# Kernel tuning notes

Hardware: AMD Instinct MI355X
Metric: run time of the kernel (lower is better)

Reference implementation:

```python
import jax, jax.numpy as jnp
import numpy as np

B, S, D_IN, D_OUT = 4, 2048, 4096, 16384


def setup_inputs() -> dict:
    key = jax.random.key(0)
    k1, k2, k3, k4 = jax.random.split(key, 4)
    x = jax.random.normal(k1, (B, S, D_IN), dtype=jnp.float32)
    # per-channel symmetric int8 weights, [out_features, in_features]
    weight_int8 = jax.random.randint(k2, (D_OUT, D_IN), -128, 128, dtype=jnp.int32).astype(jnp.int8)
    # per-channel weight scales (positive, realistic magnitude)
    weight_scale = jax.random.uniform(k3, (D_OUT,), dtype=jnp.float32) * 0.01 + 1e-4
    # static per-tensor activation scale (calibrated constant)
    act_scale = jnp.float32(0.02)
    bias = jax.random.normal(k4, (D_OUT,), dtype=jnp.float32) * 0.1
    return {"x": x, "weight_int8": weight_int8, "weight_scale": weight_scale,
            "act_scale": act_scale, "bias": bias}


def reference(x, weight_int8, weight_scale, act_scale, bias):
    orig_shape = x.shape
    orig_dtype = x.dtype
    x2d = x.reshape(-1, orig_shape[-1])  # [M, D_in]
    # static per-tensor symmetric activation quantization
    x_int8 = jnp.clip(jnp.round(x2d.astype(jnp.float32) / act_scale), -128, 127).astype(jnp.int8)
    y_int32 = jnp.matmul(x_int8, weight_int8.T, preferred_element_type=jnp.int32)  # [M, D_out]
    output_scale = (act_scale * weight_scale).astype(jnp.float32)  # [D_out]
    y = y_int32.astype(jnp.float32) * output_scale[None, :] + bias.astype(jnp.float32)[None, :]
    return y.reshape(*orig_shape[:-1], y.shape[-1]).astype(orig_dtype)
```

## Files before the change

### kernel.cpp

```cpp
#include <hip/hip_runtime.h>
#include <stdint.h>

#define GAS __attribute__((address_space(1)))
#define LAS __attribute__((address_space(3)))

typedef int v4i __attribute__((ext_vector_type(4)));

constexpr int Mdim = 8192;
constexpr int Ndim = 16384;
constexpr int Kdim = 4096;

__device__ __forceinline__ int pack4i8(int a, int b, int c, int d) {
    return (a & 255) | ((b & 255) << 8) | ((c & 255) << 16) | ((d & 255) << 24);
}

__device__ __forceinline__ int qz(float v, float inv) {
    return (int)fminf(fmaxf(rintf(v * inv), -128.0f), 127.0f);
}

__global__ void k_quant_x(const float* __restrict__ x, const float* __restrict__ asc,
                          int8_t* __restrict__ xq) {
    const int i = blockIdx.x * blockDim.x + threadIdx.x;
    const float inv = 1.0f / *asc;
    const float4* xv = (const float4*)x + (size_t)i * 4;
    float4 f0 = xv[0], f1 = xv[1], f2 = xv[2], f3 = xv[3];
    int4 o;
    o.x = pack4i8(qz(f0.x, inv), qz(f0.y, inv), qz(f0.z, inv), qz(f0.w, inv));
    o.y = pack4i8(qz(f1.x, inv), qz(f1.y, inv), qz(f1.z, inv), qz(f1.w, inv));
    o.z = pack4i8(qz(f2.x, inv), qz(f2.y, inv), qz(f2.z, inv), qz(f2.w, inv));
    o.w = pack4i8(qz(f3.x, inv), qz(f3.y, inv), qz(f3.z, inv), qz(f3.w, inv));
    ((int4*)xq)[i] = o;
}

__global__ void k_conv_w(const int* __restrict__ w, int8_t* __restrict__ wq) {
    const int i = blockIdx.x * blockDim.x + threadIdx.x;
    const int4* wv = (const int4*)w + (size_t)i * 4;
    int4 a = wv[0], b = wv[1], c = wv[2], d = wv[3];
    int4 o;
    o.x = pack4i8(a.x, a.y, a.z, a.w);
    o.y = pack4i8(b.x, b.y, b.z, b.w);
    o.z = pack4i8(c.x, c.y, c.z, c.w);
    o.w = pack4i8(d.x, d.y, d.z, d.w);
    ((int4*)wq)[i] = o;
}

constexpr int NSTEP = Kdim / 64;

__global__ __launch_bounds__(512, 2)
void k_gemm256(const int8_t* __restrict__ Aq, const int8_t* __restrict__ Bq,
               const float* __restrict__ wscale, const float* __restrict__ asc,
               const float* __restrict__ bias, float* __restrict__ out) {
    __shared__ __align__(16) int8_t lds[131072];
    const int tid = threadIdx.x, lane = tid & 63, w = tid >> 6;
    const int wm = w >> 2, wn = w & 3;
    const int lrow = lane & 15, kgrp = lane >> 4;

    const int bid = blockIdx.x;
    const int swz = ((bid & 7) << 8) | (bid >> 3);
    const int mt = swz & 31, nt = swz >> 5;
    const int m0 = mt << 8, n0 = nt << 8;

    const int srow = (w << 4) + (lane >> 2);
    const int scol = (((lane & 3) ^ ((lane >> 3) & 3)) << 4);
    const int8_t* pA0 = Aq + (size_t)(m0 + srow) * Kdim + scol;
    const int8_t* pA1 = pA0 + (size_t)128 * Kdim;
    const int8_t* pB0 = Bq + (size_t)(n0 + srow) * Kdim + scol;
    const int8_t* pB1 = pB0 + (size_t)128 * Kdim;
    const int dstoff = w << 10;

    auto stage = [&](int slot, int kb) {
        int8_t* ba = lds + (slot << 14) + dstoff;
        int8_t* bb = lds + 65536 + (slot << 14) + dstoff;
        __builtin_amdgcn_global_load_lds((const GAS void*)(pB0 + kb), (LAS void*)bb, 16, 0, 0);
        __builtin_amdgcn_global_load_lds((const GAS void*)(pB1 + kb), (LAS void*)(bb + 8192), 16, 0, 0);
        __builtin_amdgcn_global_load_lds((const GAS void*)(pA0 + kb), (LAS void*)ba, 16, 0, 0);
        __builtin_amdgcn_global_load_lds((const GAS void*)(pA1 + kb), (LAS void*)(ba + 8192), 16, 0, 0);
    };

    const int kc = (kgrp ^ ((lrow >> 1) & 3)) << 4;
    const int arowb = (((wm << 7) + lrow) << 6) + kc;
    const int browb = (((wn << 6) + lrow) << 6) + kc;

    auto readfr = [&](int slot, v4i* a, v4i* b) {
        const int8_t* As_ = lds + (slot << 14);
        const int8_t* Bs_ = lds + 65536 + (slot << 14);
#pragma unroll
        for (int f = 0; f < 4; ++f)
            b[f] = *(const v4i*)(Bs_ + browb + f * 1024);
#pragma unroll
        for (int f = 0; f < 8; ++f)
            a[f] = *(const v4i*)(As_ + arowb + f * 1024);
    };

    v4i acc[8][4];
#pragma unroll
    for (int i = 0; i < 8; ++i)
#pragma unroll
        for (int j = 0; j < 4; ++j) acc[i][j] = (v4i){0, 0, 0, 0};

    auto domfma = [&](v4i* a, v4i* b) {
        __builtin_amdgcn_s_setprio(1);
#pragma unroll
        for (int fi = 0; fi < 8; ++fi)
#pragma unroll
            for (int fj = 0; fj < 4; ++fj)
                acc[fi][fj] = __builtin_amdgcn_mfma_i32_16x16x64_i8(a[fi], b[fj], acc[fi][fj], 0, 0, 0);
        __builtin_amdgcn_s_setprio(0);
    };

    v4i aP[8], bP[4], aQ[8], bQ[4];

    stage(0, 0); stage(1, 64); stage(2, 128);
    asm volatile("s_waitcnt vmcnt(8)" ::: "memory");
    __builtin_amdgcn_s_barrier();
    readfr(0, aP, bP);

    int kb = 192;
    for (int s = 0; s < NSTEP; s += 2) {
        if (s < NSTEP - 1) {
            if (s == NSTEP - 2) asm volatile("s_waitcnt vmcnt(0)" ::: "memory");
            else                asm volatile("s_waitcnt vmcnt(4)" ::: "memory");
            __builtin_amdgcn_s_barrier();
            readfr((s + 1) & 3, aQ, bQ);
            if (s < NSTEP - 3) { stage((s + 3) & 3, kb); kb += 64; }
        }
        domfma(aP, bP);
        const int t = s + 1;
        if (t < NSTEP - 1) {
            asm volatile("s_waitcnt vmcnt(4)" ::: "memory");
            __builtin_amdgcn_s_barrier();
            readfr((t + 1) & 3, aP, bP);
            if (t < NSTEP - 3) { stage((t + 3) & 3, kb); kb += 64; }
        }
        domfma(aQ, bQ);
    }

    const float ascale = *asc;
#pragma unroll
    for (int fj = 0; fj < 4; ++fj) {
        const int col = n0 + (wn << 6) + fj * 16 + lrow;
        const float sc = ascale * wscale[col];
        const float bb = bias[col];
#pragma unroll
        for (int mi = 0; mi < 8; ++mi) {
            const int r0 = m0 + (wm << 7) + mi * 16 + (kgrp << 2);
            float* o = out + (size_t)r0 * Ndim + col;
#pragma unroll
            for (int q = 0; q < 4; ++q)
                o[(size_t)q * Ndim] = (float)acc[mi][fj][q] * sc + bb;
        }
    }
}

template <bool AQ, bool BQ>
__global__ __launch_bounds__(256)
void k_gemm(const int8_t* __restrict__ Aq, const float* __restrict__ Xf,
            const int8_t* __restrict__ Bq, const int* __restrict__ W32,
            const float* __restrict__ wscale, const float* __restrict__ asc,
            const float* __restrict__ bias, float* __restrict__ out) {
    constexpr int BM = 128, BN = 128, BK = 64;
    constexpr int KT = Kdim / BK;
    __shared__ __align__(16) int8_t As[2][BM * BK];
    __shared__ __align__(16) int8_t Bs[2][BN * BK];

    const int tid  = threadIdx.x;
    const int lane = tid & 63;
    const int wid  = tid >> 6;
    const int wm = wid >> 1, wn = wid & 1;
    const int lrow = lane & 15, kgrp = lane >> 4;

    const int cpx = gridDim.x >> 3;
    const int swz = ((int)blockIdx.x & 7) * cpx + ((int)blockIdx.x >> 3);
    const int mt = swz & (Mdim / BM - 1);
    const int nt = swz / (Mdim / BM);
    const int m0 = mt * BM, n0 = nt * BN;

    const float ascale = *asc;
    const float inv = 1.0f / ascale;

    v4i acc[4][4];
#pragma unroll
    for (int i = 0; i < 4; ++i)
#pragma unroll
        for (int j = 0; j < 4; ++j) acc[i][j] = (v4i){0, 0, 0, 0};

    auto stage = [&](int buf, int kt) {
        const int k0 = kt * BK;
        if constexpr (AQ) {
            int8_t* ldsp = &As[buf][wid << 10];
            const int8_t* g = Aq + (size_t)(m0 + (tid >> 2)) * Kdim + k0 + ((tid & 3) << 4);
            __builtin_amdgcn_global_load_lds((const GAS void*)g, (LAS void*)ldsp, 16, 0, 0);
            __builtin_amdgcn_global_load_lds((const GAS void*)(g + (size_t)64 * Kdim),
                                             (LAS void*)(ldsp + 4096), 16, 0, 0);
        } else {
            const int row = tid >> 1, cb = (tid & 1) << 5;
            const float4* src = (const float4*)(Xf + (size_t)(m0 + row) * Kdim + k0 + cb);
            int t[8];
#pragma unroll
            for (int j = 0; j < 8; ++j) {
                float4 f = src[j];
                t[j] = pack4i8(qz(f.x, inv), qz(f.y, inv), qz(f.z, inv), qz(f.w, inv));
            }
            int4* dst = (int4*)&As[buf][row * BK + cb];
            dst[0] = make_int4(t[0], t[1], t[2], t[3]);
            dst[1] = make_int4(t[4], t[5], t[6], t[7]);
        }
        if constexpr (BQ) {
            int8_t* ldsp = &Bs[buf][wid << 10];
            const int8_t* g = Bq + (size_t)(n0 + (tid >> 2)) * Kdim + k0 + ((tid & 3) << 4);
            __builtin_amdgcn_global_load_lds((const GAS void*)g, (LAS void*)ldsp, 16, 0, 0);
            __builtin_amdgcn_global_load_lds((const GAS void*)(g + (size_t)64 * Kdim),
                                             (LAS void*)(ldsp + 4096), 16, 0, 0);
        } else {
            const int row = tid >> 1, cb = (tid & 1) << 5;
            const int4* src = (const int4*)(W32 + (size_t)(n0 + row) * Kdim + k0 + cb);
            int t[8];
#pragma unroll
            for (int j = 0; j < 8; ++j) {
                int4 vv = src[j];
                t[j] = pack4i8(vv.x, vv.y, vv.z, vv.w);
            }
            int4* dst = (int4*)&Bs[buf][row * BK + cb];
            dst[0] = make_int4(t[0], t[1], t[2], t[3]);
            dst[1] = make_int4(t[4], t[5], t[6], t[7]);
        }
    };

    stage(0, 0);
    for (int kt = 0; kt < KT; ++kt) {
        const int cur = kt & 1;
        __syncthreads();
        if (kt + 1 < KT) stage(cur ^ 1, kt + 1);

        v4i a[4], b[4];
        const int koff = kgrp << 4;
#pragma unroll
        for (int i = 0; i < 4; ++i) {
            a[i] = *(const v4i*)&As[cur][(wm * 64 + i * 16 + lrow) * BK + koff];
            b[i] = *(const v4i*)&Bs[cur][(wn * 64 + i * 16 + lrow) * BK + koff];
        }
#pragma unroll
        for (int i = 0; i < 4; ++i)
#pragma unroll
            for (int j = 0; j < 4; ++j)
                acc[i][j] = __builtin_amdgcn_mfma_i32_16x16x64_i8(a[i], b[j], acc[i][j], 0, 0, 0);
    }

#pragma unroll
    for (int j = 0; j < 4; ++j) {
        const int col = n0 + wn * 64 + j * 16 + lrow;
        const float sc = ascale * wscale[col];
        const float bb = bias[col];
#pragma unroll
        for (int i = 0; i < 4; ++i) {
            const int r0 = m0 + wm * 64 + i * 16 + (kgrp << 2);
            float* o = out + (size_t)r0 * Ndim + col;
#pragma unroll
            for (int r = 0; r < 4; ++r)
                o[(size_t)r * Ndim] = (float)acc[i][j][r] * sc + bb;
        }
    }
}

extern "C" void kernel_launch(void* const* d_in, const int* in_sizes, int n_in,
                              void* d_out, int out_size, void* d_ws, size_t ws_size,
                              hipStream_t stream) {
    const float* x      = (const float*)d_in[0];
    const int*   w32    = (const int*)d_in[1];
    const float* wscale = (const float*)d_in[2];
    const float* asc    = (const float*)d_in[3];
    const float* bias   = (const float*)d_in[4];
    float* out = (float*)d_out;

    const size_t nx = (size_t)Mdim * Kdim;
    const size_t nw = (size_t)Ndim * Kdim;
    int8_t* xq = (int8_t*)d_ws;
    int8_t* wq = xq + nx;

    const bool haveX = ws_size >= nx;
    const bool haveW = ws_size >= nx + nw;

    if (haveX) k_quant_x<<<(int)(nx / 16 / 256), 256, 0, stream>>>(x, asc, xq);
    if (haveW) k_conv_w<<<(int)(nw / 16 / 256), 256, 0, stream>>>(w32, wq);

    if (haveW) {
        dim3 grid((Mdim / 256) * (Ndim / 256));
        k_gemm256<<<grid, 512, 0, stream>>>(xq, wq, wscale, asc, bias, out);
    } else if (haveX) {
        dim3 grid((Mdim / 128) * (Ndim / 128));
        k_gemm<true, false><<<grid, 256, 0, stream>>>(xq, x, wq, w32, wscale, asc, bias, out);
    } else {
        dim3 grid((Mdim / 128) * (Ndim / 128));
        k_gemm<false, false><<<grid, 256, 0, stream>>>(xq, x, wq, w32, wscale, asc, bias, out);
    }
}
```

Before: 923.9 us.

## Restructure int8 GEMM main loop into fine-grained half-tile phases with interleaved loads

Replaces the 4-slot double-fragment pipeline with an 8-phase schedule per two 128-wide K tiles. Each phase computes half of the M fragments (4x4 MFMAs) and issues one staged global-to-LDS load. It also reads only 4 A fragments at a time, which lowers register pressure. The aim is to interleave memory traffic and LDS reads more evenly with MFMA work, in the style of ping-pong schedules. The cost is two barriers per phase and hand-tuned vmcnt accounting, which may add sync overhead or risk correctness.

```diff
diff --git a/kernel.cpp b/kernel.cpp
--- a/kernel.cpp
+++ b/kernel.cpp
@@ -44,7 +44,35 @@
     ((int4*)wq)[i] = o;
 }
 
-constexpr int NSTEP = Kdim / 64;
+constexpr int NT    = Kdim / 128;
+constexpr int NITER = NT / 2;
+
+#define VM10 asm volatile("s_waitcnt vmcnt(10)" ::: "memory")
+#define VM8  asm volatile("s_waitcnt vmcnt(8)"  ::: "memory")
+#define VM4  asm volatile("s_waitcnt vmcnt(4)"  ::: "memory")
+#define VM0  asm volatile("s_waitcnt vmcnt(0)"  ::: "memory")
+
+#define PHASE(ABASE, BBASE, READB, AROW, ACC0, STAGE_STMT, VM_STMT)            \
+  {                                                                            \
+    if (READB) {                                                               \
+      _Pragma("unroll") for (int f = 0; f < 4; ++f)                            \
+          bfr[f] = *(const v4i*)(lds + (ABASE) + 32768 + browb + f * 1024);    \
+    }                                                                          \
+    _Pragma("unroll") for (int f = 0; f < 4; ++f)                              \
+        afr[f] = *(const v4i*)(lds + (ABASE) + (AROW) + f * 1024);             \
+    STAGE_STMT;                                                                \
+    VM_STMT;                                                                   \
+    __builtin_amdgcn_s_barrier();                                              \
+    asm volatile("s_waitcnt lgkmcnt(0)" ::: "memory");                         \
+    __builtin_amdgcn_sched_barrier(0);                                         \
+    __builtin_amdgcn_s_setprio(1);                                             \
+    _Pragma("unroll") for (int fi = 0; fi < 4; ++fi)                           \
+        _Pragma("unroll") for (int fj = 0; fj < 4; ++fj)                       \
+            acc[(ACC0) + fi][fj] = __builtin_amdgcn_mfma_i32_16x16x64_i8(      \
+                afr[fi], bfr[fj], acc[(ACC0) + fi][fj], 0, 0, 0);              \
+    __builtin_amdgcn_s_setprio(0);                                             \
+    __builtin_amdgcn_s_barrier();                                              \
+  }
 
 __global__ __launch_bounds__(512, 2)
 void k_gemm256(const int8_t* __restrict__ Aq, const int8_t* __restrict__ Bq,
@@ -60,37 +88,30 @@
     const int mt = swz & 31, nt = swz >> 5;
     const int m0 = mt << 8, n0 = nt << 8;
 
-    const int srow = (w << 4) + (lane >> 2);
-    const int scol = (((lane & 3) ^ ((lane >> 3) & 3)) << 4);
-    const int8_t* pA0 = Aq + (size_t)(m0 + srow) * Kdim + scol;
-    const int8_t* pA1 = pA0 + (size_t)128 * Kdim;
-    const int8_t* pB0 = Bq + (size_t)(n0 + srow) * Kdim + scol;
-    const int8_t* pB1 = pB0 + (size_t)128 * Kdim;
+    const int srow = tid >> 2;
+    const int scol = (((tid & 3) ^ ((tid >> 3) & 3)) << 4);
+    const int8_t* rowA0 = Aq + (size_t)(m0 + srow) * Kdim + scol;
+    const int8_t* rowB0 = Bq + (size_t)(n0 + srow) * Kdim + scol;
+    const size_t rb1off = (size_t)128 * Kdim;
     const int dstoff = w << 10;
 
-    auto stage = [&](int slot, int kb) {
-        int8_t* ba = lds + (slot << 14) + dstoff;
-        int8_t* bb = lds + 65536 + (slot << 14) + dstoff;
-        __builtin_amdgcn_global_load_lds((const GAS void*)(pB0 + kb), (LAS void*)bb, 16, 0, 0);
-        __builtin_amdgcn_global_load_lds((const GAS void*)(pB1 + kb), (LAS void*)(bb + 8192), 16, 0, 0);
-        __builtin_amdgcn_global_load_lds((const GAS void*)(pA0 + kb), (LAS void*)ba, 16, 0, 0);
-        __builtin_amdgcn_global_load_lds((const GAS void*)(pA1 + kb), (LAS void*)(ba + 8192), 16, 0, 0);
+    auto stA = [&](int t, int ks) {
+        int8_t* d = lds + ((t & 1) << 16) + (ks << 14) + dstoff;
+        const int8_t* s = rowA0 + t * 128 + ks * 64;
+        __builtin_amdgcn_global_load_lds((const GAS void*)s, (LAS void*)d, 16, 0, 0);
+        __builtin_amdgcn_global_load_lds((const GAS void*)(s + rb1off), (LAS void*)(d + 8192), 16, 0, 0);
     };
+    auto stB = [&](int t, int ks) {
+        int8_t* d = lds + ((t & 1) << 16) + 32768 + (ks << 14) + dstoff;
+        const int8_t* s = rowB0 + t * 128 + ks * 64;
+        __builtin_amdgcn_global_load_lds((const GAS void*)s, (LAS void*)d, 16, 0, 0);
+        __builtin_amdgcn_global_load_lds((const GAS void*)(s + rb1off), (LAS void*)(d + 8192), 16, 0, 0);
+    };
 
     const int kc = (kgrp ^ ((lrow >> 1) & 3)) << 4;
-    const int arowb = (((wm << 7) + lrow) << 6) + kc;
-    const int browb = (((wn << 6) + lrow) << 6) + kc;
-
-    auto readfr = [&](int slot, v4i* a, v4i* b) {
-        const int8_t* As_ = lds + (slot << 14);
-        const int8_t* Bs_ = lds + 65536 + (slot << 14);
-#pragma unroll
-        for (int f = 0; f < 4; ++f)
-            b[f] = *(const v4i*)(Bs_ + browb + f * 1024);
-#pragma unroll
-        for (int f = 0; f < 8; ++f)
-            a[f] = *(const v4i*)(As_ + arowb + f * 1024);
-    };
+    const int arow0 = ((wm << 7) + lrow) * 64 + kc;
+    const int arow1 = ((wm << 7) + 64 + lrow) * 64 + kc;
+    const int browb = ((wn << 6) + lrow) * 64 + kc;
 
     v4i acc[8][4];
 #pragma unroll
@@ -98,41 +119,35 @@
 #pragma unroll
         for (int j = 0; j < 4; ++j) acc[i][j] = (v4i){0, 0, 0, 0};
 
-    auto domfma = [&](v4i* a, v4i* b) {
-        __builtin_amdgcn_s_setprio(1);
-#pragma unroll
-        for (int fi = 0; fi < 8; ++fi)
-#pragma unroll
-            for (int fj = 0; fj < 4; ++fj)
-                acc[fi][fj] = __builtin_amdgcn_mfma_i32_16x16x64_i8(a[fi], b[fj], acc[fi][fj], 0, 0, 0);
-        __builtin_amdgcn_s_setprio(0);
-    };
-
-    v4i aP[8], bP[4], aQ[8], bQ[4];
-
-    stage(0, 0); stage(1, 64); stage(2, 128);
-    asm volatile("s_waitcnt vmcnt(8)" ::: "memory");
+    v4i afr[4], bfr[4];
+
+
+    stA(0, 0); stA(0, 1); stB(0, 0); stB(0, 1);
+    stA(1, 0); stB(1, 0); stB(1, 1);
+    VM0;
     __builtin_amdgcn_s_barrier();
-    readfr(0, aP, bP);
-
-    int kb = 192;
-    for (int s = 0; s < NSTEP; s += 2) {
-        if (s < NSTEP - 1) {
-            if (s == NSTEP - 2) asm volatile("s_waitcnt vmcnt(0)" ::: "memory");
-            else                asm volatile("s_waitcnt vmcnt(4)" ::: "memory");
-            __builtin_amdgcn_s_barrier();
-            readfr((s + 1) & 3, aQ, bQ);
-            if (s < NSTEP - 3) { stage((s + 3) & 3, kb); kb += 64; }
-        }
-        domfma(aP, bP);
-        const int t = s + 1;
-        if (t < NSTEP - 1) {
-            asm volatile("s_waitcnt vmcnt(4)" ::: "memory");
-            __builtin_amdgcn_s_barrier();
-            readfr((t + 1) & 3, aP, bP);
-            if (t < NSTEP - 3) { stage((t + 3) & 3, kb); kb += 64; }
-        }
-        domfma(aQ, bQ);
+
+    for (int j = 0; j < NITER - 1; ++j) {
+        const int t0 = 2 * j, t1 = 2 * j + 1;
+        PHASE(0,     0, true,  arow0, 0, stA(t1, 1),     );
+        PHASE(0,     0, false, arow1, 4, stB(t0 + 2, 0), VM10);
+        PHASE(16384, 0, true,  arow0, 0, stA(t0 + 2, 0), );
+        PHASE(16384, 0, false, arow1, 4, stB(t0 + 2, 1), VM10);
+        PHASE(65536, 0, true,  arow0, 0, stA(t0 + 2, 1), );
+        PHASE(65536, 0, false, arow1, 4, stB(t1 + 2, 0), VM10);
+        PHASE(81920, 0, true,  arow0, 0, stA(t1 + 2, 0), );
+        PHASE(81920, 0, false, arow1, 4, stB(t1 + 2, 1), VM10);
+    }
+
+    {
+        PHASE(0,     0, true,  arow0, 0, stA(31, 1), );
+        PHASE(0,     0, false, arow1, 4, ,           VM8);
+        PHASE(16384, 0, true,  arow0, 0, ,           );
+        PHASE(16384, 0, false, arow1, 4, ,           VM4);
+        PHASE(65536, 0, true,  arow0, 0, ,           );
+        PHASE(65536, 0, false, arow1, 4, ,           VM0);
+        PHASE(81920, 0, true,  arow0, 0, ,           );
+        PHASE(81920, 0, false, arow1, 4, ,           );
     }
 
     const float ascale = *asc;
```

Result: faster. 830.1 us (-10.1%).
